# Optimization experiments

Hardware: AMD Instinct MI355X
Metric: run time of the kernel (lower is better)

Reference implementation:

```python
import jax, jax.numpy as jnp
import numpy as np

P = 8192          # number of gaussians
H = 256           # image height
W = 256           # image width
TANX = 0.5        # tan(fovx/2)
TANY = 0.5        # tan(fovy/2)
SCALE_MOD = 1.0
CHUNK = 128       # gaussians composited per scan step
FX = W / (2.0 * TANX)   # focal_x, as in forward()
FY = H / (2.0 * TANY)   # focal_y


def setup_inputs() -> dict:
    key = jax.random.key(0)
    k = jax.random.split(key, 6)
    # place gaussians in the camera frustum (camera at origin, looking +z)
    z = jax.random.uniform(k[0], (P,), minval=2.0, maxval=6.0)
    xy = jax.random.normal(k[1], (P, 2)) * 0.4 * (z * TANX)[:, None]
    means3D = jnp.concatenate([xy, z[:, None]], axis=1)
    scales = 0.01 + 0.04 * jax.random.uniform(k[2], (P, 3))
    rotations = jax.random.normal(k[3], (P, 4))  # normalized inside reference
    opacities = 0.05 + 0.9 * jax.random.uniform(k[4], (P, 1))
    colors_precomp = jax.random.uniform(k[5], (P, 3))
    background = jnp.zeros((3,), jnp.float32)
    viewmatrix = jnp.eye(4, dtype=jnp.float32)  # row-vector convention: p' = [p,1] @ V
    znear, zfar = 0.01, 100.0
    Pm = np.zeros((4, 4), np.float32)
    Pm[0, 0] = 1.0 / TANX
    Pm[1, 1] = 1.0 / TANY
    Pm[2, 2] = zfar / (zfar - znear)
    Pm[2, 3] = -(zfar * znear) / (zfar - znear)
    Pm[3, 2] = 1.0
    projmatrix = jnp.asarray(Pm.T)  # row-vector convention (full proj = proj @ view, view = I)
    return dict(means3D=means3D, colors_precomp=colors_precomp, opacities=opacities,
                scales=scales, rotations=rotations, background=background,
                viewmatrix=viewmatrix, projmatrix=projmatrix)


def _quat_to_rot(q):
    q = q / jnp.linalg.norm(q, axis=-1, keepdims=True)
    r, x, y, z = q[:, 0], q[:, 1], q[:, 2], q[:, 3]
    R = jnp.stack([
        1 - 2 * (y * y + z * z), 2 * (x * y - r * z), 2 * (x * z + r * y),
        2 * (x * y + r * z), 1 - 2 * (x * x + z * z), 2 * (y * z - r * x),
        2 * (x * z - r * y), 2 * (y * z + r * x), 1 - 2 * (x * x + y * y)], axis=-1)
    return R.reshape(-1, 3, 3)


def _forward(means3D, colors_precomp, opacities, scales, rotations, background,
             viewmatrix, projmatrix):
    Pn = means3D.shape[0]
    # --- preprocess: 3D covariance from scale/rotation ---
    R = _quat_to_rot(rotations)
    s2 = (scales * SCALE_MOD) ** 2
    Sigma = jnp.einsum('pij,pj,pkj->pik', R, s2, R)  # R diag(s^2) R^T, [P,3,3]
    hom = jnp.concatenate([means3D, jnp.ones((Pn, 1), means3D.dtype)], axis=1)
    p_view = (hom @ viewmatrix)[:, :3]
    p_hom = hom @ projmatrix
    p_proj = p_hom[:, :3] / (p_hom[:, 3:4] + 1e-7)
    # NDC -> pixel centers
    mean2d = jnp.stack([((p_proj[:, 0] + 1.0) * W - 1.0) * 0.5,
                        ((p_proj[:, 1] + 1.0) * H - 1.0) * 0.5], axis=1)
    depths = p_view[:, 2]
    # --- EWA splatting: project covariance to 2D ---
    Rv = viewmatrix[:3, :3]
    cov_cam = jnp.einsum('ji,pjk,kl->pil', Rv, Sigma, Rv)  # Rv^T Sigma Rv
    tz = p_view[:, 2]
    tx = jnp.clip(p_view[:, 0] / tz, -1.3 * TANX, 1.3 * TANX) * tz
    ty = jnp.clip(p_view[:, 1] / tz, -1.3 * TANY, 1.3 * TANY) * tz
    zero = jnp.zeros_like(tz)
    J = jnp.stack([jnp.stack([FX / tz, zero, -FX * tx / tz ** 2], -1),
                   jnp.stack([zero, FY / tz, -FY * ty / tz ** 2], -1)], axis=1)  # [P,2,3]
    cov2d = jnp.einsum('pij,pjk,plk->pil', J, cov_cam, J)
    a = cov2d[:, 0, 0] + 0.3  # low-pass dilation as in 3DGS
    b = cov2d[:, 0, 1]
    c = cov2d[:, 1, 1] + 0.3
    det = a * c - b * b
    conic = jnp.stack([c, -b, a], axis=-1) / det[:, None]
    # --- global depth sort ---
    order = jnp.argsort(depths)
    m2d = mean2d[order]
    con = conic[order]
    col = colors_precomp[order]
    op = opacities[order]
    # --- per-pixel front-to-back alpha compositing ---
    px, py = jnp.meshgrid(jnp.arange(W, dtype=jnp.float32),
                          jnp.arange(H, dtype=jnp.float32))
    pixf = jnp.stack([px.ravel(), py.ravel()], axis=-1)  # [HW,2]
    n_chunks = Pn // CHUNK
    xs = (m2d.reshape(n_chunks, CHUNK, 2), con.reshape(n_chunks, CHUNK, 3),
          col.reshape(n_chunks, CHUNK, 3), op.reshape(n_chunks, CHUNK, 1))

    def step(carry, x):
        accum, T = carry
        m, cn, cl, o = x
        d = m[:, None, :] - pixf[None]  # [C,HW,2]
        power = (-0.5 * (cn[:, 0:1] * d[..., 0] ** 2 + cn[:, 2:3] * d[..., 1] ** 2)
                 - cn[:, 1:2] * d[..., 0] * d[..., 1])
        alpha = jnp.minimum(0.99, o * jnp.exp(power))
        alpha = jnp.where((power > 0.0) | (alpha < 1.0 / 255.0), 0.0, alpha)
        cp = jnp.cumprod(1.0 - alpha, axis=0)  # within-chunk transmittance
        excl = jnp.concatenate([jnp.ones((1, alpha.shape[1]), alpha.dtype), cp[:-1]], 0)
        wgt = alpha * excl * T[None]
        accum = accum + jnp.einsum('cp,cd->pd', wgt, cl)
        return (accum, T * cp[-1]), None

    accum0 = jnp.zeros((H * W, 3), jnp.float32)
    T0 = jnp.ones((H * W,), jnp.float32)
    (accum, T), _ = jax.lax.scan(step, (accum0, T0), xs)
    out = accum + T[:, None] * background[None]
    return out.reshape(H, W, 3).transpose(2, 0, 1)  # [3,H,W]


def reference(means3D, colors_precomp, opacities, scales, rotations, background,
              viewmatrix, projmatrix):
    return _forward(means3D, colors_precomp, opacities, scales, rotations,
                    background, viewmatrix, projmatrix)
```

## Files before the change

kernel.cpp:

```cpp
#include <hip/hip_runtime.h>


#define PN 8192
#define IH 256
#define IW 256


__global__ __launch_bounds__(256) void preprocess_kernel(
    const float* __restrict__ means, const float* __restrict__ colors,
    const float* __restrict__ ops, const float* __restrict__ scales,
    const float* __restrict__ rots, const float* __restrict__ V,
    const float* __restrict__ Pm, float* __restrict__ ws)
{
    int i = blockIdx.x * 256 + threadIdx.x;
    if (i >= PN) return;

    float mx3 = means[3 * i], my3 = means[3 * i + 1], mz3 = means[3 * i + 2];
    float qr = rots[4 * i], qx = rots[4 * i + 1], qy = rots[4 * i + 2], qz = rots[4 * i + 3];
    float qn = 1.0f / sqrtf(qr * qr + qx * qx + qy * qy + qz * qz);
    float r = qr * qn, x = qx * qn, y = qy * qn, z = qz * qn;

    float R00 = 1.f - 2.f * (y * y + z * z), R01 = 2.f * (x * y - r * z), R02 = 2.f * (x * z + r * y);
    float R10 = 2.f * (x * y + r * z), R11 = 1.f - 2.f * (x * x + z * z), R12 = 2.f * (y * z - r * x);
    float R20 = 2.f * (x * z - r * y), R21 = 2.f * (y * z + r * x), R22 = 1.f - 2.f * (x * x + y * y);

    float s0 = scales[3 * i];     s0 *= s0;
    float s1 = scales[3 * i + 1]; s1 *= s1;
    float s2 = scales[3 * i + 2]; s2 *= s2;

    float Sg[3][3];
    Sg[0][0] = R00 * R00 * s0 + R01 * R01 * s1 + R02 * R02 * s2;
    Sg[0][1] = R00 * R10 * s0 + R01 * R11 * s1 + R02 * R12 * s2;
    Sg[0][2] = R00 * R20 * s0 + R01 * R21 * s1 + R02 * R22 * s2;
    Sg[1][1] = R10 * R10 * s0 + R11 * R11 * s1 + R12 * R12 * s2;
    Sg[1][2] = R10 * R20 * s0 + R11 * R21 * s1 + R12 * R22 * s2;
    Sg[2][2] = R20 * R20 * s0 + R21 * R21 * s1 + R22 * R22 * s2;
    Sg[1][0] = Sg[0][1]; Sg[2][0] = Sg[0][2]; Sg[2][1] = Sg[1][2];

    float pv0 = mx3 * V[0] + my3 * V[4] + mz3 * V[8]  + V[12];
    float pv1 = mx3 * V[1] + my3 * V[5] + mz3 * V[9]  + V[13];
    float pv2 = mx3 * V[2] + my3 * V[6] + mz3 * V[10] + V[14];
    float ph0 = mx3 * Pm[0] + my3 * Pm[4] + mz3 * Pm[8]  + Pm[12];
    float ph1 = mx3 * Pm[1] + my3 * Pm[5] + mz3 * Pm[9]  + Pm[13];
    float ph3 = mx3 * Pm[3] + my3 * Pm[7] + mz3 * Pm[11] + Pm[15];
    float pw = 1.0f / (ph3 + 1e-7f);
    float m2x = ((ph0 * pw + 1.0f) * (float)IW - 1.0f) * 0.5f;
    float m2y = ((ph1 * pw + 1.0f) * (float)IH - 1.0f) * 0.5f;

    float Rv[3][3];
#pragma unroll
    for (int rr = 0; rr < 3; ++rr)
#pragma unroll
        for (int cc2 = 0; cc2 < 3; ++cc2) Rv[rr][cc2] = V[rr * 4 + cc2];
    float M[3][3];
#pragma unroll
    for (int j = 0; j < 3; ++j)
#pragma unroll
        for (int l = 0; l < 3; ++l)
            M[j][l] = Sg[j][0] * Rv[0][l] + Sg[j][1] * Rv[1][l] + Sg[j][2] * Rv[2][l];
    float cc[3][3];
#pragma unroll
    for (int ii = 0; ii < 3; ++ii)
#pragma unroll
        for (int l = 0; l < 3; ++l)
            cc[ii][l] = Rv[0][ii] * M[0][l] + Rv[1][ii] * M[1][l] + Rv[2][ii] * M[2][l];

    const float FX = 256.0f, FY = 256.0f;
    float tz = pv2;
    float itz = 1.0f / tz;
    float limx = 0.65f, limy = 0.65f;
    float txz = fminf(fmaxf(pv0 * itz, -limx), limx);
    float tyz = fminf(fmaxf(pv1 * itz, -limy), limy);
    float tx = txz * tz, ty = tyz * tz;
    float J00 = FX * itz, J02 = -FX * tx * itz * itz;
    float J11 = FY * itz, J12 = -FY * ty * itz * itz;

    float u00 = J00 * cc[0][0] + J02 * cc[2][0];
    float u01 = J00 * cc[0][1] + J02 * cc[2][1];
    float u02 = J00 * cc[0][2] + J02 * cc[2][2];
    float u11 = J11 * cc[1][1] + J12 * cc[2][1];
    float u12 = J11 * cc[1][2] + J12 * cc[2][2];
    float cov00 = u00 * J00 + u02 * J02;
    float cov01 = u01 * J11 + u02 * J12;
    float cov11 = u11 * J11 + u12 * J12;

    float a = cov00 + 0.3f;
    float b = cov01;
    float c = cov11 + 0.3f;
    float det = a * c - b * b;
    float idet = 1.0f / det;
    float cA = c * idet;
    float cB = -b * idet;
    float cC = a * idet;

    float ex = sqrtf(11.2f * a);
    float ey = sqrtf(11.2f * c);
    int x0 = max(0,  (int)floorf((m2x - ex) * 0.125f));
    int x1 = min(31, (int)floorf((m2x + ex) * 0.125f));
    int y0 = max(0,  (int)floorf((m2y - ey) * 0.125f));
    int y1 = min(31, (int)floorf((m2y + ey) * 0.125f));
    x0 = min(x0, 31); y0 = min(y0, 31); x1 = max(x1, 0); y1 = max(y1, 0);
    unsigned box = (unsigned)x0 | ((unsigned)x1 << 8) | ((unsigned)y0 << 16) | ((unsigned)y1 << 24);

    ws[i] = pv2;
    float4* preA = (float4*)(ws + PN);
    float4* preB = (float4*)(ws + 5 * PN);
    preA[i] = make_float4(m2x, m2y, cA, cB);
    preB[i] = make_float4(cC, ops[i], colors[3 * i], colors[3 * i + 1]);
    ws[9 * PN + i] = colors[3 * i + 2];
    ((unsigned*)(ws + 10 * PN))[i] = box;
}

__global__ __launch_bounds__(256) void sort_scatter_kernel(float* __restrict__ ws)
{
    const float* dep = ws;
    const float4* d4 = (const float4*)ws;
    int lane = threadIdx.x & 63;
    int wid = threadIdx.x >> 6;
    int gbase = blockIdx.x * 16 + wid * 4;

    float di0 = dep[gbase], di1 = dep[gbase + 1], di2 = dep[gbase + 2], di3 = dep[gbase + 3];
    int r0 = 0, r1 = 0, r2 = 0, r3 = 0;
#pragma unroll 4
    for (int k = 0; k < 32; ++k) {
        int j4 = k * 64 + lane;
        float4 d = d4[j4];
        int jb = j4 * 4;
        r0 += (d.x < di0) || (d.x == di0 && (jb    ) < gbase);
        r0 += (d.y < di0) || (d.y == di0 && (jb + 1) < gbase);
        r0 += (d.z < di0) || (d.z == di0 && (jb + 2) < gbase);
        r0 += (d.w < di0) || (d.w == di0 && (jb + 3) < gbase);
        r1 += (d.x < di1) || (d.x == di1 && (jb    ) < gbase + 1);
        r1 += (d.y < di1) || (d.y == di1 && (jb + 1) < gbase + 1);
        r1 += (d.z < di1) || (d.z == di1 && (jb + 2) < gbase + 1);
        r1 += (d.w < di1) || (d.w == di1 && (jb + 3) < gbase + 1);
        r2 += (d.x < di2) || (d.x == di2 && (jb    ) < gbase + 2);
        r2 += (d.y < di2) || (d.y == di2 && (jb + 1) < gbase + 2);
        r2 += (d.z < di2) || (d.z == di2 && (jb + 2) < gbase + 2);
        r2 += (d.w < di2) || (d.w == di2 && (jb + 3) < gbase + 2);
        r3 += (d.x < di3) || (d.x == di3 && (jb    ) < gbase + 3);
        r3 += (d.y < di3) || (d.y == di3 && (jb + 1) < gbase + 3);
        r3 += (d.z < di3) || (d.z == di3 && (jb + 2) < gbase + 3);
        r3 += (d.w < di3) || (d.w == di3 && (jb + 3) < gbase + 3);
    }
#pragma unroll
    for (int off = 1; off < 64; off <<= 1) {
        r0 += __shfl_xor(r0, off);
        r1 += __shfl_xor(r1, off);
        r2 += __shfl_xor(r2, off);
        r3 += __shfl_xor(r3, off);
    }
    if (lane < 4) {
        int rk = (lane == 0) ? r0 : (lane == 1) ? r1 : (lane == 2) ? r2 : r3;
        int i = gbase + lane;
        const float4* preA = (const float4*)(ws + PN);
        const float4* preB = (const float4*)(ws + 5 * PN);
        float4* sA = (float4*)(ws + 11 * PN);
        float4* sB = (float4*)(ws + 15 * PN);
        sA[rk] = preA[i];
        sB[rk] = preB[i];
        ws[19 * PN + rk] = ws[9 * PN + i];
        ((unsigned*)(ws + 20 * PN))[rk] = ((const unsigned*)(ws + 10 * PN))[i];
    }
}

__global__ __launch_bounds__(256) void raster_kernel(
    const float* __restrict__ ws, const float* __restrict__ bg,
    float* __restrict__ out)
{
    __shared__ float4 lsA[4][256];
    __shared__ float4 lsB[4][256];
    __shared__ float  lsb[4][256];
    volatile __shared__ float waveT[4];

    int tid = threadIdx.x;
    int lane = tid & 63, w = tid >> 6;
    int tileIdx = (blockIdx.x * 97) & 1023;
    int tileX = tileIdx & 31, tileY = tileIdx >> 5;
    int px = tileX * 8 + (lane & 7), py = tileY * 8 + (lane >> 3);
    float pxf = (float)px, pyf = (float)py;

    const float4* sA = (const float4*)(ws + 11 * PN);
    const float4* sB = (const float4*)(ws + 15 * PN);
    const float* sb = ws + 19 * PN;
    const unsigned* sbox = (const unsigned*)(ws + 20 * PN);

    if (tid < 4) waveT[tid] = 1.0f;
    __syncthreads();

    float T = 1.0f, ar = 0.0f, ag = 0.0f, ab = 0.0f;

    int c0 = w * 8;
    unsigned bx[4];
#pragma unroll
    for (int k = 0; k < 4; ++k) bx[k] = sbox[c0 * 256 + k * 64 + lane];

    bool dead = false;
    for (int chunk = c0; chunk < c0 + 8 && !dead; ++chunk) {
        float pre = 1.0f;
        for (int q = 0; q < w; ++q) pre *= waveT[q];
        if (pre < 1e-4f) break;

        unsigned long long wv[4];
#pragma unroll
        for (int k = 0; k < 4; ++k) {
            bool ov = (tileX >= (int)(bx[k] & 255)) & (tileX <= (int)((bx[k] >> 8) & 255)) &
                      (tileY >= (int)((bx[k] >> 16) & 255)) & (tileY <= (int)(bx[k] >> 24));
            wv[k] = __ballot(ov);
        }
        if (chunk + 1 < c0 + 8) {
#pragma unroll
            for (int k = 0; k < 4; ++k) bx[k] = sbox[(chunk + 1) * 256 + k * 64 + lane];
        }
        if (!(wv[0] | wv[1] | wv[2] | wv[3])) continue;

        int base = chunk * 256;
        int cnt = 0;
#pragma unroll
        for (int k = 0; k < 4; ++k) {
            unsigned long long wk = wv[k];
            if ((wk >> lane) & 1ull) {
                int slot = cnt + (int)__popcll(wk & ((1ull << lane) - 1ull));
                int g = base + k * 64 + lane;
                lsA[w][slot] = sA[g];
                lsB[w][slot] = sB[g];
                lsb[w][slot] = sb[g];
            }
            cnt += (int)__popcll(wk);
        }
        asm volatile("s_waitcnt lgkmcnt(0)" ::: "memory");

        for (int j = 0; j < cnt; ++j) {
            if (w > 0 && (j & 15) == 15) {
                float p2 = 1.0f;
                for (int q = 0; q < w; ++q) p2 *= waveT[q];
                if (p2 < 1e-4f) { dead = true; break; }
            }
            float4 A = lsA[w][j];
            float4 B = lsB[w][j];
            float bcol = lsb[w][j];
            float dx = A.x - pxf, dy = A.y - pyf;
            float power = -0.5f * (A.z * dx * dx + B.x * dy * dy) - A.w * dx * dy;
            float alpha = fminf(0.99f, B.y * __expf(power));
            bool skip = (power > 0.0f) | (alpha < (1.0f / 255.0f));
            float a2 = skip ? 0.0f : alpha;
            float wgt = a2 * T;
            ar = fmaf(wgt, B.z, ar);
            ag = fmaf(wgt, B.w, ag);
            ab = fmaf(wgt, bcol, ab);
            T *= (1.0f - a2);
        }
        asm volatile("s_waitcnt lgkmcnt(0)" ::: "memory");

        if (__all(T < 1e-5f)) break;

        float tmax = T;
#pragma unroll
        for (int off = 1; off < 64; off <<= 1) tmax = fmaxf(tmax, __shfl_xor(tmax, off));
        if (lane == 0) waveT[w] = tmax;
    }

    lsb[w][lane * 4 + 0] = ar;
    lsb[w][lane * 4 + 1] = ag;
    lsb[w][lane * 4 + 2] = ab;
    lsb[w][lane * 4 + 3] = T;
    __syncthreads();

    if (w == 0) {
        float A0 = 0.f, A1 = 0.f, A2 = 0.f, Tt = 1.f;
#pragma unroll
        for (int q = 0; q < 4; ++q) {
            A0 += Tt * lsb[q][lane * 4 + 0];
            A1 += Tt * lsb[q][lane * 4 + 1];
            A2 += Tt * lsb[q][lane * 4 + 2];
            Tt *= lsb[q][lane * 4 + 3];
        }
        int pidx = py * IW + px;
        out[pidx]               = A0 + Tt * bg[0];
        out[IH * IW + pidx]     = A1 + Tt * bg[1];
        out[2 * IH * IW + pidx] = A2 + Tt * bg[2];
    }
}

extern "C" void kernel_launch(void* const* d_in, const int* in_sizes, int n_in,
                              void* d_out, int out_size, void* d_ws, size_t ws_size,
                              hipStream_t stream) {
    const float* means  = (const float*)d_in[0];
    const float* colors = (const float*)d_in[1];
    const float* ops    = (const float*)d_in[2];
    const float* scales = (const float*)d_in[3];
    const float* rots   = (const float*)d_in[4];
    const float* bg     = (const float*)d_in[5];
    const float* viewm  = (const float*)d_in[6];
    const float* projm  = (const float*)d_in[7];
    float* out = (float*)d_out;
    float* ws  = (float*)d_ws;

    hipLaunchKernelGGL(preprocess_kernel, dim3(PN / 256), dim3(256), 0, stream,
                       means, colors, ops, scales, rots, viewm, projm, ws);
    hipLaunchKernelGGL(sort_scatter_kernel, dim3(PN / 16), dim3(256), 0, stream, ws);
    hipLaunchKernelGGL(raster_kernel, dim3(1024), dim3(256), 0, stream, ws, bg, out);
}
```

Baseline: 117.6 us.

## Use persistent raster blocks with atomic tile ticket in center-first order

The raster kernel becomes persistent: each block repeatedly takes a tile index from a global atomic ticket and looks it up in a tile-order table. Preprocess builds that table by sorting tiles by distance from the image centre, so the dense centre tiles are handed out first and load balances better. The change also drops the prefetch of the next chunk's boxes and the mid-chunk early-exit check on earlier waves. It adds a memset, atomics and per-tile block-wide syncs, and the grid stays at 1024 blocks, so whether blocks actually loop over several tiles depends on scheduling.

After: 124.6 us. 6.0% more time.

```diff
diff --git a/kernel.cpp b/kernel.cpp
--- a/kernel.cpp
+++ b/kernel.cpp
@@ -5,6 +5,9 @@
 #define IH 256
 #define IW 256
 
+
+#define WS_TICKET (21 * PN)
+#define WS_ORDER  (21 * PN + 64)
 
 __global__ __launch_bounds__(256) void preprocess_kernel(
     const float* __restrict__ means, const float* __restrict__ colors,
@@ -109,6 +112,24 @@
     preB[i] = make_float4(cC, ops[i], colors[3 * i], colors[3 * i + 1]);
     ws[9 * PN + i] = colors[3 * i + 2];
     ((unsigned*)(ws + 10 * PN))[i] = box;
+
+    {
+        int t = i >> 3, s = i & 7;
+        float tcx = (float)((t & 31) * 8) - 124.0f;
+        float tcy = (float)((t >> 5) * 8) - 124.0f;
+        float d2 = tcx * tcx + tcy * tcy;
+        int cnt = 0;
+        int u0 = s * 128;
+        for (int u = u0; u < u0 + 128; ++u) {
+            float ux = (float)((u & 31) * 8) - 124.0f;
+            float uy = (float)((u >> 5) * 8) - 124.0f;
+            float du = ux * ux + uy * uy;
+            cnt += (du < d2) || (du == d2 && u < t);
+        }
+#pragma unroll
+        for (int off = 1; off < 8; off <<= 1) cnt += __shfl_xor(cnt, off);
+        if (s == 0) ((unsigned*)(ws + WS_ORDER))[cnt] = (unsigned)t;
+    }
 }
 
 __global__ __launch_bounds__(256) void sort_scatter_kernel(float* __restrict__ ws)
@@ -165,120 +186,116 @@
 }
 
 __global__ __launch_bounds__(256) void raster_kernel(
-    const float* __restrict__ ws, const float* __restrict__ bg,
+    float* __restrict__ ws, const float* __restrict__ bg,
     float* __restrict__ out)
 {
     __shared__ float4 lsA[4][256];
     __shared__ float4 lsB[4][256];
     __shared__ float  lsb[4][256];
     volatile __shared__ float waveT[4];
+    __shared__ int curT;
 
     int tid = threadIdx.x;
     int lane = tid & 63, w = tid >> 6;
-    int tileIdx = (blockIdx.x * 97) & 1023;
-    int tileX = tileIdx & 31, tileY = tileIdx >> 5;
-    int px = tileX * 8 + (lane & 7), py = tileY * 8 + (lane >> 3);
-    float pxf = (float)px, pyf = (float)py;
 
     const float4* sA = (const float4*)(ws + 11 * PN);
     const float4* sB = (const float4*)(ws + 15 * PN);
     const float* sb = ws + 19 * PN;
     const unsigned* sbox = (const unsigned*)(ws + 20 * PN);
-
-    if (tid < 4) waveT[tid] = 1.0f;
-    __syncthreads();
-
-    float T = 1.0f, ar = 0.0f, ag = 0.0f, ab = 0.0f;
-
-    int c0 = w * 8;
-    unsigned bx[4];
-#pragma unroll
-    for (int k = 0; k < 4; ++k) bx[k] = sbox[c0 * 256 + k * 64 + lane];
-
-    bool dead = false;
-    for (int chunk = c0; chunk < c0 + 8 && !dead; ++chunk) {
-        float pre = 1.0f;
-        for (int q = 0; q < w; ++q) pre *= waveT[q];
-        if (pre < 1e-4f) break;
-
-        unsigned long long wv[4];
-#pragma unroll
-        for (int k = 0; k < 4; ++k) {
-            bool ov = (tileX >= (int)(bx[k] & 255)) & (tileX <= (int)((bx[k] >> 8) & 255)) &
-                      (tileY >= (int)((bx[k] >> 16) & 255)) & (tileY <= (int)(bx[k] >> 24));
-            wv[k] = __ballot(ov);
+    unsigned* ticket = (unsigned*)(ws + WS_TICKET);
+    const unsigned* orderTab = (const unsigned*)(ws + WS_ORDER);
+
+    for (;;) {
+        if (tid == 0) curT = (int)atomicAdd(ticket, 1u);
+        if (tid < 4) waveT[tid] = 1.0f;
+        __syncthreads();
+        int tk = curT;
+        if (tk >= 1024) break;
+
+        int tileIdx = (int)orderTab[tk];
+        int tileX = tileIdx & 31, tileY = tileIdx >> 5;
+        int px = tileX * 8 + (lane & 7), py = tileY * 8 + (lane >> 3);
+        float pxf = (float)px, pyf = (float)py;
+
+        float T = 1.0f, ar = 0.0f, ag = 0.0f, ab = 0.0f;
+
+        for (int chunk = w * 8; chunk < w * 8 + 8; ++chunk) {
+            float pre = 1.0f;
+            for (int q = 0; q < w; ++q) pre *= waveT[q];
+            if (pre < 1e-4f) break;
+
+            int base = chunk * 256;
+            unsigned long long wv[4];
+#pragma unroll
+            for (int k = 0; k < 4; ++k) {
+                unsigned bx = sbox[base + k * 64 + lane];
+                bool ov = (tileX >= (int)(bx & 255)) & (tileX <= (int)((bx >> 8) & 255)) &
+                          (tileY >= (int)((bx >> 16) & 255)) & (tileY <= (int)(bx >> 24));
+                wv[k] = __ballot(ov);
+            }
+            if (!(wv[0] | wv[1] | wv[2] | wv[3])) continue;
+
+            int cnt = 0;
+#pragma unroll
+            for (int k = 0; k < 4; ++k) {
+                unsigned long long wk = wv[k];
+                if ((wk >> lane) & 1ull) {
+                    int slot = cnt + (int)__popcll(wk & ((1ull << lane) - 1ull));
+                    int g = base + k * 64 + lane;
+                    lsA[w][slot] = sA[g];
+                    lsB[w][slot] = sB[g];
+                    lsb[w][slot] = sb[g];
+                }
+                cnt += (int)__popcll(wk);
+            }
+            asm volatile("s_waitcnt lgkmcnt(0)" ::: "memory");
+
+            for (int j = 0; j < cnt; ++j) {
+                float4 A = lsA[w][j];
+                float4 B = lsB[w][j];
+                float bcol = lsb[w][j];
+                float dx = A.x - pxf, dy = A.y - pyf;
+                float power = -0.5f * (A.z * dx * dx + B.x * dy * dy) - A.w * dx * dy;
+                float alpha = fminf(0.99f, B.y * __expf(power));
+                bool skip = (power > 0.0f) | (alpha < (1.0f / 255.0f));
+                float a2 = skip ? 0.0f : alpha;
+                float wgt = a2 * T;
+                ar = fmaf(wgt, B.z, ar);
+                ag = fmaf(wgt, B.w, ag);
+                ab = fmaf(wgt, bcol, ab);
+                T *= (1.0f - a2);
+            }
+            asm volatile("s_waitcnt lgkmcnt(0)" ::: "memory");
+
+            if (__all(T < 1e-5f)) break;
+
+            float tmax = T;
+#pragma unroll
+            for (int off = 1; off < 64; off <<= 1) tmax = fmaxf(tmax, __shfl_xor(tmax, off));
+            if (lane == 0) waveT[w] = tmax;
         }
-        if (chunk + 1 < c0 + 8) {
-#pragma unroll
-            for (int k = 0; k < 4; ++k) bx[k] = sbox[(chunk + 1) * 256 + k * 64 + lane];
+
+        lsb[w][lane * 4 + 0] = ar;
+        lsb[w][lane * 4 + 1] = ag;
+        lsb[w][lane * 4 + 2] = ab;
+        lsb[w][lane * 4 + 3] = T;
+        __syncthreads();
+
+        if (w == 0) {
+            float A0 = 0.f, A1 = 0.f, A2 = 0.f, Tt = 1.f;
+#pragma unroll
+            for (int q = 0; q < 4; ++q) {
+                A0 += Tt * lsb[q][lane * 4 + 0];
+                A1 += Tt * lsb[q][lane * 4 + 1];
+                A2 += Tt * lsb[q][lane * 4 + 2];
+                Tt *= lsb[q][lane * 4 + 3];
+            }
+            int pidx = py * IW + px;
+            out[pidx]               = A0 + Tt * bg[0];
+            out[IH * IW + pidx]     = A1 + Tt * bg[1];
+            out[2 * IH * IW + pidx] = A2 + Tt * bg[2];
         }
-        if (!(wv[0] | wv[1] | wv[2] | wv[3])) continue;
-
-        int base = chunk * 256;
-        int cnt = 0;
-#pragma unroll
-        for (int k = 0; k < 4; ++k) {
-            unsigned long long wk = wv[k];
-            if ((wk >> lane) & 1ull) {
-                int slot = cnt + (int)__popcll(wk & ((1ull << lane) - 1ull));
-                int g = base + k * 64 + lane;
-                lsA[w][slot] = sA[g];
-                lsB[w][slot] = sB[g];
-                lsb[w][slot] = sb[g];
-            }
-            cnt += (int)__popcll(wk);
-        }
-        asm volatile("s_waitcnt lgkmcnt(0)" ::: "memory");
-
-        for (int j = 0; j < cnt; ++j) {
-            if (w > 0 && (j & 15) == 15) {
-                float p2 = 1.0f;
-                for (int q = 0; q < w; ++q) p2 *= waveT[q];
-                if (p2 < 1e-4f) { dead = true; break; }
-            }
-            float4 A = lsA[w][j];
-            float4 B = lsB[w][j];
-            float bcol = lsb[w][j];
-            float dx = A.x - pxf, dy = A.y - pyf;
-            float power = -0.5f * (A.z * dx * dx + B.x * dy * dy) - A.w * dx * dy;
-            float alpha = fminf(0.99f, B.y * __expf(power));
-            bool skip = (power > 0.0f) | (alpha < (1.0f / 255.0f));
-            float a2 = skip ? 0.0f : alpha;
-            float wgt = a2 * T;
-            ar = fmaf(wgt, B.z, ar);
-            ag = fmaf(wgt, B.w, ag);
-            ab = fmaf(wgt, bcol, ab);
-            T *= (1.0f - a2);
-        }
-        asm volatile("s_waitcnt lgkmcnt(0)" ::: "memory");
-
-        if (__all(T < 1e-5f)) break;
-
-        float tmax = T;
-#pragma unroll
-        for (int off = 1; off < 64; off <<= 1) tmax = fmaxf(tmax, __shfl_xor(tmax, off));
-        if (lane == 0) waveT[w] = tmax;
-    }
-
-    lsb[w][lane * 4 + 0] = ar;
-    lsb[w][lane * 4 + 1] = ag;
-    lsb[w][lane * 4 + 2] = ab;
-    lsb[w][lane * 4 + 3] = T;
-    __syncthreads();
-
-    if (w == 0) {
-        float A0 = 0.f, A1 = 0.f, A2 = 0.f, Tt = 1.f;
-#pragma unroll
-        for (int q = 0; q < 4; ++q) {
-            A0 += Tt * lsb[q][lane * 4 + 0];
-            A1 += Tt * lsb[q][lane * 4 + 1];
-            A2 += Tt * lsb[q][lane * 4 + 2];
-            Tt *= lsb[q][lane * 4 + 3];
-        }
-        int pidx = py * IW + px;
-        out[pidx]               = A0 + Tt * bg[0];
-        out[IH * IW + pidx]     = A1 + Tt * bg[1];
-        out[2 * IH * IW + pidx] = A2 + Tt * bg[2];
+        __syncthreads();
     }
 }
 
@@ -296,6 +313,7 @@
     float* out = (float*)d_out;
     float* ws  = (float*)d_ws;
 
+    hipMemsetAsync((char*)d_ws + WS_TICKET * 4, 0, 4, stream);
     hipLaunchKernelGGL(preprocess_kernel, dim3(PN / 256), dim3(256), 0, stream,
                        means, colors, ops, scales, rots, viewm, projm, ws);
     hipLaunchKernelGGL(sort_scatter_kernel, dim3(PN / 16), dim3(256), 0, stream, ws);
```
